# Kernel tuning notes

Measured on AMD Instinct MI355X. Metric: run time of the kernel, lower is better.

Reference implementation:

```python
import jax, jax.numpy as jnp
import numpy as np

D_FIELDS = 16
HIDDEN = 16
N_POINTS = 1_000_000


def setup_inputs() -> dict:
    key = jax.random.key(0)
    ks = jax.random.split(key, 7)
    x = jax.random.normal(ks[0], (1, 3, N_POINTS), dtype=jnp.float32)
    # stacked per-field Conv1d(k=1) weights: conv weight [out,in,1] -> matrix [out,in]
    W1 = jax.random.normal(ks[1], (D_FIELDS, HIDDEN, 3), dtype=jnp.float32) * 0.1
    b1 = jax.random.normal(ks[2], (D_FIELDS, HIDDEN), dtype=jnp.float32) * 0.1
    W2 = jax.random.normal(ks[3], (D_FIELDS, HIDDEN, HIDDEN), dtype=jnp.float32) * 0.1
    b2 = jax.random.normal(ks[4], (D_FIELDS, HIDDEN), dtype=jnp.float32) * 0.1
    W3 = jax.random.normal(ks[5], (D_FIELDS, 3, HIDDEN), dtype=jnp.float32) * 0.1
    b3 = jax.random.normal(ks[6], (D_FIELDS, 3), dtype=jnp.float32) * 0.1
    return {"x": x, "W1": W1, "b1": b1, "W2": W2, "b2": b2, "W3": W3, "b3": b3, "D": D_FIELDS}


def reference(x, W1, b1, W2, b2, W3, b3, D):
    # x: [1, 3, N]. Original loops d in range(D) applying field d's MLP to x and
    # concatenating along dim 0 -> [D, 3, N]. Fused here as batched GEMMs over d.
    xs = x[0]  # [3, N]
    h = jax.nn.relu(jnp.einsum('dhc,cn->dhn', W1, xs) + b1[:, :, None])      # [D,H,N]
    h = jax.nn.relu(jnp.einsum('dgh,dhn->dgn', W2, h) + b2[:, :, None])      # [D,H,N]
    out = jnp.einsum('doh,dhn->don', W3, h) + b3[:, :, None]                 # [D,3,N]
    return out
```

## Files before the change

kernel.cpp:

```cpp
#include <hip/hip_runtime.h>


#define MFMA16(a, b, c) __builtin_amdgcn_mfma_f32_16x16x16f16((a), (b), (c), 0, 0, 0)

#define TILES_PER_WAVE 5
#define WAVES_PER_BLOCK 4
#define PTS_PER_BLOCK (TILES_PER_WAVE * WAVES_PER_BLOCK * 16)

typedef __fp16 pk16x2 __attribute__((ext_vector_type(2)));
typedef _Float16 half4_t __attribute__((ext_vector_type(4)));
typedef float float4_t __attribute__((ext_vector_type(4)));

union H2I { pk16x2 h; int i; };
union Frag { half4_t v; int i[2]; };

__device__ __forceinline__ int pkrtz(float a, float b) {
    H2I u; u.h = __builtin_amdgcn_cvt_pkrtz(a, b); return u.i;
}

__global__ __launch_bounds__(256) void fields_mfma16_kernel(
    const float* __restrict__ x,
    const float* __restrict__ W1, const float* __restrict__ b1,
    const float* __restrict__ W2, const float* __restrict__ b2,
    const float* __restrict__ W3, const float* __restrict__ b3,
    float* __restrict__ out, int N)
{
    __shared__ __align__(16) _Float16 A1c[16][16][4];
    __shared__ __align__(16) _Float16 A2c[16][16][16];
    __shared__ __align__(16) _Float16 A3c[16][16][16];
    __shared__ __align__(16) float B1c[16][16];
    __shared__ __align__(16) float B2c[16][16];
    __shared__ __align__(16) float B3c[16][16];

    {
        const int td = threadIdx.x;
        const int d = td >> 4, m = td & 15;
        const float* w1 = W1 + (d * 16 + m) * 3;
        A1c[d][m][0] = (_Float16)w1[0];
        A1c[d][m][1] = (_Float16)w1[1];
        A1c[d][m][2] = (_Float16)w1[2];
        A1c[d][m][3] = (_Float16)0.f;
        const float* w2 = W2 + (d * 16 + m) * 16;
#pragma unroll
        for (int k = 0; k < 16; ++k) A2c[d][m][k] = (_Float16)w2[k];
        if (m < 3) {
            const float* w3 = W3 + (d * 3 + m) * 16;
#pragma unroll
            for (int k = 0; k < 16; ++k) A3c[d][m][k] = (_Float16)w3[k];
        } else {
#pragma unroll
            for (int k = 0; k < 16; ++k) A3c[d][m][k] = (_Float16)0.f;
        }
        B1c[d][m] = b1[d * 16 + m];
        B2c[d][m] = b2[d * 16 + m];
        B3c[d][m] = (m < 3) ? b3[d * 3 + m] : 0.f;
    }
    __syncthreads();

    const int lane = threadIdx.x & 63;
    const int wave = threadIdx.x >> 6;
    const int q = lane >> 4;
    const int n16 = lane & 15;

    const int base = blockIdx.x * PTS_PER_BLOCK + wave * (TILES_PER_WAVE * 16);

    Frag xf[TILES_PER_WAVE];
#pragma unroll
    for (int t = 0; t < TILES_PER_WAVE; ++t) {
        const int pt = base + t * 16 + n16;
        float x0 = 0.f, x1 = 0.f, x2 = 0.f;
        if (q == 0 && pt < N) {
            x0 = x[pt];
            x1 = x[(size_t)N + pt];
            x2 = x[2 * (size_t)N + pt];
        }
        xf[t].i[0] = pkrtz(x0, x1);
        xf[t].i[1] = pkrtz(x2, 0.f);
    }

#pragma unroll 1
    for (int d = 0; d < 16; ++d) {
        Frag a1, a2, a3;
        a1.v = *(const half4_t*)&A1c[d][n16][0];
        a2.v = *(const half4_t*)&A2c[d][n16][q * 4];
        a3.v = *(const half4_t*)&A3c[d][n16][q * 4];
        const float4_t bias1 = *(const float4_t*)&B1c[d][q * 4];
        const float4_t bias2 = *(const float4_t*)&B2c[d][q * 4];
        const float4_t bias3 = *(const float4_t*)&B3c[d][q * 4];

#pragma unroll
        for (int t = 0; t < TILES_PER_WAVE; ++t) {
            float4_t acc = bias1;
            acc = MFMA16(a1.v, xf[t].v, acc);
            Frag bf;
            bf.i[0] = pkrtz(fmaxf(acc.x, 0.f), fmaxf(acc.y, 0.f));
            bf.i[1] = pkrtz(fmaxf(acc.z, 0.f), fmaxf(acc.w, 0.f));
            acc = bias2;
            acc = MFMA16(a2.v, bf.v, acc);
            Frag cf;
            cf.i[0] = pkrtz(fmaxf(acc.x, 0.f), fmaxf(acc.y, 0.f));
            cf.i[1] = pkrtz(fmaxf(acc.z, 0.f), fmaxf(acc.w, 0.f));
            acc = bias3;
            acc = MFMA16(a3.v, cf.v, acc);
            const int pt = base + t * 16 + n16;
            if (q == 0 && pt < N) {
                out[(size_t)(d * 3 + 0) * N + pt] = acc.x;
                out[(size_t)(d * 3 + 1) * N + pt] = acc.y;
                out[(size_t)(d * 3 + 2) * N + pt] = acc.z;
            }
        }
    }
}

extern "C" void kernel_launch(void* const* d_in, const int* in_sizes, int n_in,
                              void* d_out, int out_size, void* d_ws, size_t ws_size,
                              hipStream_t stream) {
    const float* x  = (const float*)d_in[0];
    const float* W1 = (const float*)d_in[1];
    const float* b1 = (const float*)d_in[2];
    const float* W2 = (const float*)d_in[3];
    const float* b2 = (const float*)d_in[4];
    const float* W3 = (const float*)d_in[5];
    const float* b3 = (const float*)d_in[6];
    float* out = (float*)d_out;

    const int N = in_sizes[0] / 3;
    const int grid = (N + PTS_PER_BLOCK - 1) / PTS_PER_BLOCK;
    fields_mfma16_kernel<<<grid, 256, 0, stream>>>(x, W1, b1, W2, b2, W3, b3, out, N);
}
```

Before: 251.1 us.

## Assign one field per block and load weights directly into registers

Each block now handles a single field d and one point chunk, giving a grid that is 16x larger, instead of looping over all 16 fields per block. Weights and biases go straight from global memory into MFMA fragments, so the shared-memory staging and the __syncthreads are gone. The cost is that x is reread 16 times, once per field, and there are many more blocks. Tiles per wave drop from 5 to 4.

New measurement: 288.0 us. +14.7%, slower.

```diff
diff --git a/kernel.cpp b/kernel.cpp
--- a/kernel.cpp
+++ b/kernel.cpp
@@ -3,7 +3,7 @@
 
 #define MFMA16(a, b, c) __builtin_amdgcn_mfma_f32_16x16x16f16((a), (b), (c), 0, 0, 0)
 
-#define TILES_PER_WAVE 5
+#define TILES_PER_WAVE 4
 #define WAVES_PER_BLOCK 4
 #define PTS_PER_BLOCK (TILES_PER_WAVE * WAVES_PER_BLOCK * 16)
 
@@ -18,51 +18,46 @@
     H2I u; u.h = __builtin_amdgcn_cvt_pkrtz(a, b); return u.i;
 }
 
-__global__ __launch_bounds__(256) void fields_mfma16_kernel(
+__global__ __launch_bounds__(256) void fields_fixedd_kernel(
     const float* __restrict__ x,
     const float* __restrict__ W1, const float* __restrict__ b1,
     const float* __restrict__ W2, const float* __restrict__ b2,
     const float* __restrict__ W3, const float* __restrict__ b3,
     float* __restrict__ out, int N)
 {
-    __shared__ __align__(16) _Float16 A1c[16][16][4];
-    __shared__ __align__(16) _Float16 A2c[16][16][16];
-    __shared__ __align__(16) _Float16 A3c[16][16][16];
-    __shared__ __align__(16) float B1c[16][16];
-    __shared__ __align__(16) float B2c[16][16];
-    __shared__ __align__(16) float B3c[16][16];
-
-    {
-        const int td = threadIdx.x;
-        const int d = td >> 4, m = td & 15;
-        const float* w1 = W1 + (d * 16 + m) * 3;
-        A1c[d][m][0] = (_Float16)w1[0];
-        A1c[d][m][1] = (_Float16)w1[1];
-        A1c[d][m][2] = (_Float16)w1[2];
-        A1c[d][m][3] = (_Float16)0.f;
-        const float* w2 = W2 + (d * 16 + m) * 16;
-#pragma unroll
-        for (int k = 0; k < 16; ++k) A2c[d][m][k] = (_Float16)w2[k];
-        if (m < 3) {
-            const float* w3 = W3 + (d * 3 + m) * 16;
-#pragma unroll
-            for (int k = 0; k < 16; ++k) A3c[d][m][k] = (_Float16)w3[k];
-        } else {
-#pragma unroll
-            for (int k = 0; k < 16; ++k) A3c[d][m][k] = (_Float16)0.f;
-        }
-        B1c[d][m] = b1[d * 16 + m];
-        B2c[d][m] = b2[d * 16 + m];
-        B3c[d][m] = (m < 3) ? b3[d * 3 + m] : 0.f;
-    }
-    __syncthreads();
-
     const int lane = threadIdx.x & 63;
     const int wave = threadIdx.x >> 6;
-    const int q = lane >> 4;
-    const int n16 = lane & 15;
+    const int q    = lane >> 4;
+    const int n16  = lane & 15;
 
-    const int base = blockIdx.x * PTS_PER_BLOCK + wave * (TILES_PER_WAVE * 16);
+    const int d     = blockIdx.x & 15;
+    const int chunk = blockIdx.x >> 4;
+    const int base  = chunk * PTS_PER_BLOCK + wave * (TILES_PER_WAVE * 16);
+
+    Frag a1, a2, a3;
+    {
+        const float* w1 = W1 + (d * 16 + n16) * 3;
+        a1.v = (half4_t){(_Float16)w1[0], (_Float16)w1[1], (_Float16)w1[2],
+                         (_Float16)0.f};
+        const float4_t w2 = *(const float4_t*)(W2 + (d * 16 + n16) * 16 + q * 4);
+        a2.v = (half4_t){(_Float16)w2.x, (_Float16)w2.y, (_Float16)w2.z,
+                         (_Float16)w2.w};
+        if (n16 < 3) {
+            const float4_t w3 = *(const float4_t*)(W3 + (d * 3 + n16) * 16 + q * 4);
+            a3.v = (half4_t){(_Float16)w3.x, (_Float16)w3.y, (_Float16)w3.z,
+                             (_Float16)w3.w};
+        } else {
+            a3.i[0] = 0; a3.i[1] = 0;
+        }
+    }
+    const float4_t bias1 = *(const float4_t*)(b1 + d * 16 + q * 4);
+    const float4_t bias2 = *(const float4_t*)(b2 + d * 16 + q * 4);
+    float4_t bias3 = (float4_t){0.f, 0.f, 0.f, 0.f};
+    if (q == 0) {
+        bias3.x = b3[d * 3 + 0];
+        bias3.y = b3[d * 3 + 1];
+        bias3.z = b3[d * 3 + 2];
+    }
 
     Frag xf[TILES_PER_WAVE];
 #pragma unroll
@@ -78,36 +73,26 @@
         xf[t].i[1] = pkrtz(x2, 0.f);
     }
 
-#pragma unroll 1
-    for (int d = 0; d < 16; ++d) {
-        Frag a1, a2, a3;
-        a1.v = *(const half4_t*)&A1c[d][n16][0];
-        a2.v = *(const half4_t*)&A2c[d][n16][q * 4];
-        a3.v = *(const half4_t*)&A3c[d][n16][q * 4];
-        const float4_t bias1 = *(const float4_t*)&B1c[d][q * 4];
-        const float4_t bias2 = *(const float4_t*)&B2c[d][q * 4];
-        const float4_t bias3 = *(const float4_t*)&B3c[d][q * 4];
+    float* o0 = out + (size_t)(d * 3 + 0) * N;
+    float* o1 = out + (size_t)(d * 3 + 1) * N;
+    float* o2 = out + (size_t)(d * 3 + 2) * N;
 
 #pragma unroll
-        for (int t = 0; t < TILES_PER_WAVE; ++t) {
-            float4_t acc = bias1;
-            acc = MFMA16(a1.v, xf[t].v, acc);
-            Frag bf;
-            bf.i[0] = pkrtz(fmaxf(acc.x, 0.f), fmaxf(acc.y, 0.f));
-            bf.i[1] = pkrtz(fmaxf(acc.z, 0.f), fmaxf(acc.w, 0.f));
-            acc = bias2;
-            acc = MFMA16(a2.v, bf.v, acc);
-            Frag cf;
-            cf.i[0] = pkrtz(fmaxf(acc.x, 0.f), fmaxf(acc.y, 0.f));
-            cf.i[1] = pkrtz(fmaxf(acc.z, 0.f), fmaxf(acc.w, 0.f));
-            acc = bias3;
-            acc = MFMA16(a3.v, cf.v, acc);
-            const int pt = base + t * 16 + n16;
-            if (q == 0 && pt < N) {
-                out[(size_t)(d * 3 + 0) * N + pt] = acc.x;
-                out[(size_t)(d * 3 + 1) * N + pt] = acc.y;
-                out[(size_t)(d * 3 + 2) * N + pt] = acc.z;
-            }
+    for (int t = 0; t < TILES_PER_WAVE; ++t) {
+        float4_t acc = MFMA16(a1.v, xf[t].v, bias1);
+        Frag bf;
+        bf.i[0] = pkrtz(fmaxf(acc.x, 0.f), fmaxf(acc.y, 0.f));
+        bf.i[1] = pkrtz(fmaxf(acc.z, 0.f), fmaxf(acc.w, 0.f));
+        acc = MFMA16(a2.v, bf.v, bias2);
+        Frag cf;
+        cf.i[0] = pkrtz(fmaxf(acc.x, 0.f), fmaxf(acc.y, 0.f));
+        cf.i[1] = pkrtz(fmaxf(acc.z, 0.f), fmaxf(acc.w, 0.f));
+        acc = MFMA16(a3.v, cf.v, bias3);
+        const int pt = base + t * 16 + n16;
+        if (q == 0 && pt < N) {
+            o0[pt] = acc.x;
+            o1[pt] = acc.y;
+            o2[pt] = acc.z;
         }
     }
 }
@@ -125,6 +110,7 @@
     float* out = (float*)d_out;
 
     const int N = in_sizes[0] / 3;
-    const int grid = (N + PTS_PER_BLOCK - 1) / PTS_PER_BLOCK;
-    fields_mfma16_kernel<<<grid, 256, 0, stream>>>(x, W1, b1, W2, b2, W3, b3, out, N);
+    const int chunks = (N + PTS_PER_BLOCK - 1) / PTS_PER_BLOCK;
+    const int grid = chunks * 16;
+    fields_fixedd_kernel<<<grid, 256, 0, stream>>>(x, W1, b1, W2, b2, W3, b3, out, N);
 }
```
